# Kernel tuning notes

Measured on AMD Instinct MI355X. Metric: run time of the kernel, lower is better.

Reference implementation:

```python
import jax, jax.numpy as jnp
import numpy as np
from jax.ops import segment_sum

N = 100000   # nodes
E = 1600000  # edges
D = 128      # input feature dim
H = 128      # hidden dim
S = 64       # substructure ids
G = 512      # graphs in batch
EPS = 1e-5


def setup_inputs() -> dict:
    key = jax.random.key(0)
    ks = jax.random.split(key, 12)
    subst_ids = jax.random.randint(ks[0], (N,), 0, S)
    x = jax.random.normal(ks[1], (N, D), dtype=jnp.float32)
    # column 5 carries the integer substructure id, as in data.x[:, 5].long()
    x = x.at[:, 5].set(subst_ids.astype(jnp.float32))
    edge_index = jax.random.randint(ks[2], (2, E), 0, N)
    batch = jnp.sort(jax.random.randint(ks[3], (N,), 0, G))
    s = 0.05  # weight scale to keep activations sane
    return {
        "x": x,
        "edge_index": edge_index,
        "subst_ids": subst_ids,
        "batch": batch,
        "attn_w1": jax.random.normal(ks[4], (D, 64), jnp.float32) * s,
        "attn_b1": jnp.zeros((64,), jnp.float32),
        "attn_w2": jax.random.normal(ks[5], (64, 1), jnp.float32) * s,
        "conv_w0": jax.random.normal(ks[6], (D + 1, H), jnp.float32) * s,
        "conv_b0": jnp.zeros((H,), jnp.float32),
        "conv_w1": jax.random.normal(ks[7], (H, H), jnp.float32) * s,
        "conv_b1": jnp.zeros((H,), jnp.float32),
        "conv_w2": jax.random.normal(ks[8], (H, H), jnp.float32) * s,
        "conv_b2": jnp.zeros((H,), jnp.float32),
        "conv_w3": jax.random.normal(ks[9], (H, H), jnp.float32) * s,
        "conv_b3": jnp.zeros((H,), jnp.float32),
        "bn_gamma": jnp.ones((4, H), jnp.float32),
        "bn_beta": jnp.zeros((4, H), jnp.float32),
        "bn_rmean": jnp.zeros((4, H), jnp.float32),
        "bn_rvar": jnp.ones((4, H), jnp.float32),
        "head_w1": jax.random.normal(ks[10], (H, H // 2), jnp.float32) * s,
        "head_b1": jnp.zeros((H // 2,), jnp.float32),
        "head_w2": jax.random.normal(ks[11], (H // 2, 1), jnp.float32) * s,
        "head_b2": jnp.zeros((1,), jnp.float32),
    }


def _gcn_conv(x, src, dst, dinv, w, b):
    # PyG GCNConv with self-loops: out[dst] += d^-1/2_src d^-1/2_dst (xW)[src]
    h = x @ w                                   # [N, H]
    coef = dinv[src] * dinv[dst]                # [E]
    agg = segment_sum(h[src] * coef[:, None], dst, num_segments=N)
    agg = agg + h * (dinv * dinv)[:, None]      # self-loop term
    return agg + b


def reference(x, edge_index, subst_ids, batch,
              attn_w1, attn_b1, attn_w2,
              conv_w0, conv_b0, conv_w1, conv_b1, conv_w2, conv_b2, conv_w3, conv_b3,
              bn_gamma, bn_beta, bn_rmean, bn_rvar,
              head_w1, head_b1, head_w2, head_b2):
    # --- substructure attention ---
    ones_n = jnp.ones((N,), x.dtype)
    cnt = jnp.maximum(segment_sum(ones_n, subst_ids, num_segments=S), 1.0)
    subst_mean = segment_sum(x, subst_ids, num_segments=S) / cnt[:, None]  # [S, D]
    scores = jnp.tanh(subst_mean @ attn_w1 + attn_b1) @ attn_w2            # [S, 1]
    subst_attn = jax.nn.softmax(scores, axis=0)                            # [S, 1]
    atom_attn = subst_attn[subst_ids]                                      # [N, 1]
    h = jnp.concatenate([x, atom_attn], axis=1)                            # [N, D+1]

    # --- shared symmetric normalization (self-loops included) ---
    src, dst = edge_index[0], edge_index[1]
    deg = segment_sum(jnp.ones((E,), x.dtype), dst, num_segments=N) + 1.0
    dinv = jax.lax.rsqrt(deg)

    convs = [(conv_w0, conv_b0), (conv_w1, conv_b1), (conv_w2, conv_b2), (conv_w3, conv_b3)]
    for i, (w, b) in enumerate(convs):
        h = _gcn_conv(h, src, dst, dinv, w, b)
        # BatchNorm1d in eval mode
        h = (h - bn_rmean[i]) * jax.lax.rsqrt(bn_rvar[i] + EPS) * bn_gamma[i] + bn_beta[i]
        h = jax.nn.elu(h) if i < 3 else jax.nn.relu(h)
        # dropout p=0.3 is identity in inference

    # --- global mean pool over graphs ---
    gcnt = jnp.maximum(segment_sum(jnp.ones((N,), x.dtype), batch, num_segments=G), 1.0)
    pooled = segment_sum(h, batch, num_segments=G) / gcnt[:, None]         # [G, H]

    # --- prediction head (dropout off) ---
    z = jax.nn.elu(pooled @ head_w1 + head_b1)
    return z @ head_w2 + head_b2                                            # [G, 1]
```

## Files before the change

kernel.cpp:

```cpp
#include <hip/hip_runtime.h>
#include <cmath>

#define NN 100000
#define EE 1600000
#define DD 128
#define HH 128
#define SS 64
#define GG 512

typedef float f32x4 __attribute__((ext_vector_type(4)));
typedef short s16x8 __attribute__((ext_vector_type(8)));

constexpr size_t alignup(size_t x){ return (x + 255) & ~(size_t)255; }
constexpr size_t SZ_P16   = (size_t)NN*64*sizeof(unsigned);
constexpr size_t OFF_HW   = 0;
constexpr size_t OFF_H    = alignup(OFF_HW + SZ_P16);
constexpr size_t OFF_CSRS = alignup(OFF_H + SZ_P16);
constexpr size_t OFF_ROW  = alignup(OFF_CSRS + (size_t)EE*4);
constexpr size_t OFF_RANK = alignup(OFF_ROW + (size_t)(NN+1)*4);
constexpr size_t OFF_DINV = alignup(OFF_RANK + (size_t)EE*4);
constexpr size_t OFF_BSUM = alignup(OFF_DINV + (size_t)NN*4);
constexpr size_t OFF_BOFF = alignup(OFF_BSUM + 512*4);
constexpr size_t OFF_SATT = alignup(OFF_BOFF + 512*4);
constexpr size_t OFF_GST  = alignup(OFF_SATT + 64*4);
constexpr size_t OFF_BH   = alignup(OFF_GST + 513*4);
constexpr size_t OFF_BO   = alignup(OFF_BH + (size_t)64*400*4);
constexpr size_t OFF_TOT  = alignup(OFF_BO + (size_t)64*400*4);
constexpr size_t OFF_ROW2 = alignup(OFF_TOT + 64*4);
constexpr size_t OFF_LIST = alignup(OFF_ROW2 + 65*4);
constexpr size_t OFF_W16  = alignup(OFF_LIST + (size_t)NN*4);
constexpr size_t OFF_DEG  = alignup(OFF_W16 + (size_t)3*8192*4);
constexpr size_t OFF_POOL = alignup(OFF_DEG + (size_t)NN*4);
constexpr size_t OFF_GSUM = alignup(OFF_POOL + (size_t)GG*HH*4);
constexpr size_t OFF_END  = alignup(OFF_GSUM + (size_t)SS*DD*4);
constexpr size_t ZERO_BEG   = OFF_DEG;
constexpr size_t ZERO_BYTES = OFF_END - OFF_DEG;

__device__ __forceinline__ unsigned pack2bf(float a, float b){
  unsigned ua = __float_as_uint(a); ua += 0x7fffu + ((ua >> 16) & 1u);
  unsigned ub = __float_as_uint(b); ub += 0x7fffu + ((ub >> 16) & 1u);
  return (ua >> 16) | (ub & 0xffff0000u);
}
__device__ __forceinline__ float bf_lo(unsigned u){ return __uint_as_float(u << 16); }
__device__ __forceinline__ float bf_hi(unsigned u){ return __uint_as_float(u & 0xffff0000u); }
__device__ __forceinline__ s16x8 as_s16x8(uint4 v){ union { uint4 u; s16x8 s; } x; x.u = v; return x.s; }

__global__ __launch_bounds__(256) void hist_kernel(const int* __restrict__ sid, int* __restrict__ bhist)
{
  __shared__ int h[64];
  int t = threadIdx.x, b = blockIdx.x;
  if (t < 64) h[t] = 0;
  __syncthreads();
  int n = b*256 + t;
  if (n < NN) atomicAdd(&h[sid[n]], 1);
  __syncthreads();
  if (t < 64) bhist[t*400 + b] = h[t];
}

__global__ __launch_bounds__(512) void offs_kernel(const int* __restrict__ bhist, int* __restrict__ boff2, int* __restrict__ tots)
{
  __shared__ int sh[512];
  int s = blockIdx.x, t = threadIdx.x;
  int v = (t < 391) ? bhist[s*400 + t] : 0;
  sh[t] = v;
  __syncthreads();
  for (int off = 1; off < 512; off <<= 1) {
    int u = (t >= off) ? sh[t - off] : 0;
    __syncthreads();
    sh[t] += u;
    __syncthreads();
  }
  if (t < 391) boff2[s*400 + t] = sh[t] - v;
  if (t == 511) tots[s] = sh[511];
}

__global__ __launch_bounds__(64) void base_kernel(const int* __restrict__ tots, int* __restrict__ row2)
{
  int l = threadIdx.x;
  int v = tots[l];
  int xv = v;
  #pragma unroll
  for (int off = 1; off < 64; off <<= 1) {
    int u = __shfl_up(xv, off, 64);
    if (l >= off) xv += u;
  }
  row2[l] = xv - v;
  if (l == 63) row2[64] = xv;
}

__global__ __launch_bounds__(256) void fill2_kernel(
    const int* __restrict__ sid, const int* __restrict__ row2,
    const int* __restrict__ boff2, unsigned* __restrict__ list)
{
  __shared__ int h[64];
  int t = threadIdx.x, b = blockIdx.x;
  if (t < 64) h[t] = 0;
  __syncthreads();
  int n = b*256 + t;
  if (n < NN) {
    int s = sid[n];
    int lr = atomicAdd(&h[s], 1);
    int pos = row2[s] + boff2[s*400 + b] + lr;
    list[pos] = ((unsigned)s << 24) | (unsigned)n;
  }
}

__global__ __launch_bounds__(256) void subst_sum(
    const unsigned* __restrict__ list, const float* __restrict__ x,
    float* __restrict__ gsum)
{
  int b = blockIdx.x, t = threadIdx.x;
  int lane = t & 63, w = t >> 6;
  const int per = (NN + 1023)/1024;
  const int q   = (per + 3)/4;
  int bend = min(b*per + per, NN);
  int beg = b*per + w*q;
  int end = min(bend, beg + q);
  if (beg >= end) return;
  int d0 = lane * 2;
  float ax = 0.f, ay = 0.f;
  int scur = (int)(list[beg] >> 24);
  int i = beg;
  for (; i + 4 <= end; i += 4) {
    unsigned u0 = list[i], u1 = list[i+1], u2 = list[i+2], u3 = list[i+3];
    float2 v0 = *(const float2*)(x + (size_t)(u0 & 0xffffffu)*DD + d0);
    float2 v1 = *(const float2*)(x + (size_t)(u1 & 0xffffffu)*DD + d0);
    float2 v2 = *(const float2*)(x + (size_t)(u2 & 0xffffffu)*DD + d0);
    float2 v3 = *(const float2*)(x + (size_t)(u3 & 0xffffffu)*DD + d0);
    int s0 = u0 >> 24, s1 = u1 >> 24, s2 = u2 >> 24, s3 = u3 >> 24;
    if (s0 != scur) { atomicAdd(&gsum[scur*DD + d0], ax); atomicAdd(&gsum[scur*DD + d0 + 1], ay); scur = s0; ax = 0.f; ay = 0.f; }
    ax += v0.x; ay += v0.y;
    if (s1 != scur) { atomicAdd(&gsum[scur*DD + d0], ax); atomicAdd(&gsum[scur*DD + d0 + 1], ay); scur = s1; ax = 0.f; ay = 0.f; }
    ax += v1.x; ay += v1.y;
    if (s2 != scur) { atomicAdd(&gsum[scur*DD + d0], ax); atomicAdd(&gsum[scur*DD + d0 + 1], ay); scur = s2; ax = 0.f; ay = 0.f; }
    ax += v2.x; ay += v2.y;
    if (s3 != scur) { atomicAdd(&gsum[scur*DD + d0], ax); atomicAdd(&gsum[scur*DD + d0 + 1], ay); scur = s3; ax = 0.f; ay = 0.f; }
    ax += v3.x; ay += v3.y;
  }
  for (; i < end; ++i) {
    unsigned u = list[i];
    float2 v = *(const float2*)(x + (size_t)(u & 0xffffffu)*DD + d0);
    int s = u >> 24;
    if (s != scur) { atomicAdd(&gsum[scur*DD + d0], ax); atomicAdd(&gsum[scur*DD + d0 + 1], ay); scur = s; ax = 0.f; ay = 0.f; }
    ax += v.x; ay += v.y;
  }
  atomicAdd(&gsum[scur*DD + d0],     ax);
  atomicAdd(&gsum[scur*DD + d0 + 1], ay);
}

__global__ __launch_bounds__(64) void attn_kernel(
    const float* __restrict__ g_sum, const int* __restrict__ row2,
    const float* __restrict__ w1, const float* __restrict__ b1,
    const float* __restrict__ w2, float* __restrict__ subst_attn)
{
  __shared__ float mean[SS*130];
  __shared__ float sc[SS];
  __shared__ float es[SS];
  int t = threadIdx.x;
  for (int i = t; i < SS*DD; i += 64) {
    int s = i >> 7, d = i & 127;
    float c = fmaxf((float)(row2[s+1] - row2[s]), 1.0f);
    mean[s*130 + d] = g_sum[i] / c;
  }
  __syncthreads();
  float score = 0.0f;
  for (int j = 0; j < 64; ++j) {
    float a0 = 0, a1 = 0, a2 = 0, a3 = 0;
    for (int d = 0; d < DD; d += 4) {
      a0 += mean[t*130 + d    ] * w1[(d    )*64 + j];
      a1 += mean[t*130 + d + 1] * w1[(d + 1)*64 + j];
      a2 += mean[t*130 + d + 2] * w1[(d + 2)*64 + j];
      a3 += mean[t*130 + d + 3] * w1[(d + 3)*64 + j];
    }
    score += tanhf(a0 + a1 + a2 + a3 + b1[j]) * w2[j];
  }
  sc[t] = score;
  __syncthreads();
  float m = -1e30f;
  for (int i = 0; i < SS; ++i) m = fmaxf(m, sc[i]);
  float e = expf(score - m);
  es[t] = e;
  __syncthreads();
  float sum = 0.0f;
  for (int i = 0; i < SS; ++i) sum += es[i];
  subst_attn[t] = e / sum;
}

__global__ __launch_bounds__(256) void deg_rank_kernel(
    const int* __restrict__ dst, int* __restrict__ deg, int* __restrict__ rank)
{
  int e = blockIdx.x*256 + threadIdx.x;
  if (e < EE) rank[e] = atomicAdd(&deg[dst[e]], 1);
}

__global__ __launch_bounds__(256) void dinv_kernel(const int* __restrict__ deg, float* __restrict__ dinv)
{
  int n = blockIdx.x*256 + threadIdx.x;
  if (n < NN) dinv[n] = rsqrtf((float)(deg[n] + 1));
}

__global__ __launch_bounds__(256) void scan1(const int* __restrict__ deg, int* __restrict__ row_off, int* __restrict__ bsum)
{
  __shared__ int s[256];
  int tid = threadIdx.x;
  int n = blockIdx.x*256 + tid;
  int v = (n < NN) ? deg[n] : 0;
  s[tid] = v;
  __syncthreads();
  for (int off = 1; off < 256; off <<= 1) {
    int t = (tid >= off) ? s[tid - off] : 0;
    __syncthreads();
    s[tid] += t;
    __syncthreads();
  }
  if (n < NN) row_off[n] = s[tid] - v;
  if (tid == 255) bsum[blockIdx.x] = s[255];
}

__global__ __launch_bounds__(512) void scan2(const int* __restrict__ bsum, int* __restrict__ boff, int nb)
{
  __shared__ int s[512];
  int t = threadIdx.x;
  int v = (t < nb) ? bsum[t] : 0;
  s[t] = v;
  __syncthreads();
  for (int off = 1; off < 512; off <<= 1) {
    int u = (t >= off) ? s[t - off] : 0;
    __syncthreads();
    s[t] += u;
    __syncthreads();
  }
  boff[t] = s[t] - v;
}

__global__ __launch_bounds__(256) void scan3(int* __restrict__ row_off, const int* __restrict__ boff)
{
  int n = blockIdx.x*256 + threadIdx.x;
  if (n < NN) row_off[n] = row_off[n] + boff[n >> 8];
  if (n == 0) row_off[NN] = EE;
}

__global__ __launch_bounds__(256) void fill_kernel(
    const int* __restrict__ src, const int* __restrict__ dst,
    const int* __restrict__ rank, const int* __restrict__ row_off,
    int* __restrict__ csr_src)
{
  int e = blockIdx.x*256 + threadIdx.x;
  if (e >= EE) return;
  int d = dst[e];
  int pos = row_off[d] + rank[e];
  csr_src[pos] = src[e];
}

__global__ __launch_bounds__(256) void gemm_kernel(
    const float* __restrict__ A, const float* __restrict__ W,
    unsigned* __restrict__ out,
    const int* __restrict__ sid, const float* __restrict__ sattn, int layer0)
{
  __shared__ float sA[32][129];
  __shared__ float sW[32][128];
  __shared__ float sExtra[128];
  __shared__ float sAttn[128];
  int tid = threadIdx.x;
  int tx = tid & 15, ty = tid >> 4;
  int row0 = blockIdx.x * 128;

  if (layer0) {
    if (tid < 128) sExtra[tid] = W[128*128 + tid];
    if (tid < 128) {
      int n = row0 + tid;
      sAttn[tid] = (n < NN) ? sattn[sid[n]] : 0.0f;
    }
  }

  float acc[8][8];
  #pragma unroll
  for (int i = 0; i < 8; ++i)
    #pragma unroll
    for (int j = 0; j < 8; ++j) acc[i][j] = 0.0f;

  for (int k0 = 0; k0 < 128; k0 += 32) {
    __syncthreads();
    #pragma unroll
    for (int p = 0; p < 4; ++p) {
      int q  = tid + 256*p;
      int r  = q >> 3;
      int kk = (q & 7) << 2;
      int n = row0 + r;
      float4 v = make_float4(0.f, 0.f, 0.f, 0.f);
      if (n < NN) v = *(const float4*)(A + (size_t)n*128 + k0 + kk);
      sA[kk+0][r] = v.x; sA[kk+1][r] = v.y; sA[kk+2][r] = v.z; sA[kk+3][r] = v.w;
    }
    #pragma unroll
    for (int p = 0; p < 4; ++p) {
      int q  = tid + 256*p;
      int kr = q >> 5;
      int c  = (q & 31) << 2;
      float4 v = *(const float4*)(W + (size_t)(k0 + kr)*128 + c);
      *(float4*)&sW[kr][c] = v;
    }
    __syncthreads();
    #pragma unroll 4
    for (int kk = 0; kk < 32; ++kk) {
      float av[8], wv[8];
      #pragma unroll
      for (int i = 0; i < 8; ++i) av[i] = sA[kk][ty*8 + i];
      #pragma unroll
      for (int j = 0; j < 8; ++j) wv[j] = sW[kk][tx*8 + j];
      #pragma unroll
      for (int i = 0; i < 8; ++i)
        #pragma unroll
        for (int j = 0; j < 8; ++j)
          acc[i][j] += av[i] * wv[j];
    }
  }

  if (layer0) {
    #pragma unroll
    for (int i = 0; i < 8; ++i) {
      float a = sAttn[ty*8 + i];
      #pragma unroll
      for (int j = 0; j < 8; ++j) acc[i][j] += a * sExtra[tx*8 + j];
    }
  }

  #pragma unroll
  for (int i = 0; i < 8; ++i) {
    int n = row0 + ty*8 + i;
    if (n < NN) {
      uint4 pk;
      pk.x = pack2bf(acc[i][0], acc[i][1]);
      pk.y = pack2bf(acc[i][2], acc[i][3]);
      pk.z = pack2bf(acc[i][4], acc[i][5]);
      pk.w = pack2bf(acc[i][6], acc[i][7]);
      *(uint4*)(out + (size_t)n*64 + tx*4) = pk;
    }
  }
}

__global__ __launch_bounds__(256) void packw_kernel(const float* __restrict__ W, unsigned* __restrict__ W16)
{
  int q = blockIdx.x*256 + threadIdx.x;
  int c = q & 127, kp = q >> 7;
  float f0 = W[(size_t)(2*kp  )*128 + c];
  float f1 = W[(size_t)(2*kp+1)*128 + c];
  W16[c*64 + kp] = pack2bf(f0, f1);
}

__global__ __launch_bounds__(256) void gemm16_kernel(
    const unsigned* __restrict__ A16, const unsigned* __restrict__ W16,
    unsigned* __restrict__ out)
{
  __shared__ unsigned lds[16384];
  int tid = threadIdx.x;
  int lane = tid & 63;
  int row0 = blockIdx.x * 128;

  #pragma unroll
  for (int p = 0; p < 8; ++p) {
    int q  = tid + 256*p;
    int r  = q >> 4;
    int ch = q & 15;
    int n = row0 + r;
    uint4 v = make_uint4(0u,0u,0u,0u);
    if (n < NN) v = *(const uint4*)(A16 + (size_t)n*64 + ch*4);
    int idx = (r*64 + ch*4) ^ ((r & 7) << 2);
    *(uint4*)&lds[idx] = v;
  }
  {
    const uint4* w4 = (const uint4*)W16;
    #pragma unroll
    for (int p = 0; p < 8; ++p) {
      int ch = tid + 256*p;
      int base = ch*4;
      int c = base >> 6;
      int idx = 8192 + (base ^ ((c & 7) << 2));
      *(uint4*)&lds[idx] = w4[ch];
    }
  }
  __syncthreads();

  int w = tid >> 6;
  int wrow = w * 32;
  int swz = (lane & 7) << 2;
  int kgrp = (lane >> 4) * 4;

  f32x4 acc0[8], acc1[8];
  #pragma unroll
  for (int j = 0; j < 8; ++j) { acc0[j] = (f32x4){0,0,0,0}; acc1[j] = (f32x4){0,0,0,0}; }

  #pragma unroll
  for (int kk = 0; kk < 4; ++kk) {
    int kbase = kk*16 + kgrp;
    int rowA0 = wrow + (lane & 15);
    int rowA1 = wrow + 16 + (lane & 15);
    uint4 avu0 = *(const uint4*)&lds[(rowA0*64 + kbase) ^ swz];
    uint4 avu1 = *(const uint4*)&lds[(rowA1*64 + kbase) ^ swz];
    s16x8 a0 = as_s16x8(avu0);
    s16x8 a1 = as_s16x8(avu1);
    #pragma unroll
    for (int j = 0; j < 8; ++j) {
      int col = j*16 + (lane & 15);
      uint4 bvu = *(const uint4*)&lds[8192 + ((col*64 + kbase) ^ swz)];
      s16x8 bfr = as_s16x8(bvu);
      acc0[j] = __builtin_amdgcn_mfma_f32_16x16x32_bf16(a0, bfr, acc0[j], 0, 0, 0);
      acc1[j] = __builtin_amdgcn_mfma_f32_16x16x32_bf16(a1, bfr, acc1[j], 0, 0, 0);
    }
  }
  __syncthreads();

  #pragma unroll
  for (int i2 = 0; i2 < 2; ++i2) {
    #pragma unroll
    for (int j = 0; j < 8; ++j) {
      f32x4 v = i2 ? acc1[j] : acc0[j];
      #pragma unroll
      for (int reg = 0; reg < 4; ++reg) {
        float own = v[reg];
        float part = __shfl_xor(own, 1, 64);
        if ((lane & 1) == 0) {
          int r  = wrow + i2*16 + (lane >> 4)*4 + reg;
          int cp = j*8 + ((lane & 15) >> 1);
          lds[r*68 + cp] = pack2bf(own, part);
        }
      }
    }
  }
  __syncthreads();

  #pragma unroll
  for (int p = 0; p < 8; ++p) {
    int q  = tid + 256*p;
    int r  = q >> 4;
    int ch = q & 15;
    int n = row0 + r;
    if (n < NN) {
      uint4 v = *(const uint4*)&lds[r*68 + ch*4];
      *(uint4*)(out + (size_t)n*64 + ch*4) = v;
    }
  }
}

__global__ __launch_bounds__(256) void gather_kernel(
    const unsigned* __restrict__ hw, const int* __restrict__ row_off,
    const int* __restrict__ csr_src,
    const float* __restrict__ dinv, const float* __restrict__ bias,
    const float* __restrict__ gma, const float* __restrict__ bta,
    const float* __restrict__ rmn, const float* __restrict__ rvr,
    unsigned* __restrict__ out, int relu_act)
{
  int w = (blockIdx.x*256 + threadIdx.x) >> 6;
  int lane = threadIdx.x & 63;
  int n0 = w * 2;
  if (n0 >= NN) return;
  n0 = __builtin_amdgcn_readfirstlane(n0);
  int n1 = n0 + 1;
  int j0 = lane * 2;

  float di0 = dinv[n0], di1 = dinv[n1];
  unsigned su0 = hw[(size_t)n0*64 + lane];
  unsigned su1 = hw[(size_t)n1*64 + lane];
  float ax0 = bf_lo(su0)*di0*di0, ay0 = bf_hi(su0)*di0*di0;
  float ax1 = bf_lo(su1)*di1*di1, ay1 = bf_hi(su1)*di1*di1;

  int b0 = __builtin_amdgcn_readfirstlane(row_off[n0]);
  int e0 = __builtin_amdgcn_readfirstlane(row_off[n0+1]);
  int e1 = __builtin_amdgcn_readfirstlane(row_off[n1+1]);
  int i0 = b0, i1 = e0;

  for (; i0 + 4 <= e0 && i1 + 4 <= e1; i0 += 4, i1 += 4) {
    int s00 = csr_src[i0+0], s01 = csr_src[i0+1], s02 = csr_src[i0+2], s03 = csr_src[i0+3];
    int s10 = csr_src[i1+0], s11 = csr_src[i1+1], s12 = csr_src[i1+2], s13 = csr_src[i1+3];
    unsigned u00 = hw[(size_t)s00*64 + lane];
    unsigned u01 = hw[(size_t)s01*64 + lane];
    unsigned u02 = hw[(size_t)s02*64 + lane];
    unsigned u03 = hw[(size_t)s03*64 + lane];
    unsigned u10 = hw[(size_t)s10*64 + lane];
    unsigned u11 = hw[(size_t)s11*64 + lane];
    unsigned u12 = hw[(size_t)s12*64 + lane];
    unsigned u13 = hw[(size_t)s13*64 + lane];
    float c00 = dinv[s00]*di0, c01 = dinv[s01]*di0, c02 = dinv[s02]*di0, c03 = dinv[s03]*di0;
    float c10 = dinv[s10]*di1, c11 = dinv[s11]*di1, c12 = dinv[s12]*di1, c13 = dinv[s13]*di1;
    ax0 += bf_lo(u00)*c00 + bf_lo(u01)*c01 + bf_lo(u02)*c02 + bf_lo(u03)*c03;
    ay0 += bf_hi(u00)*c00 + bf_hi(u01)*c01 + bf_hi(u02)*c02 + bf_hi(u03)*c03;
    ax1 += bf_lo(u10)*c10 + bf_lo(u11)*c11 + bf_lo(u12)*c12 + bf_lo(u13)*c13;
    ay1 += bf_hi(u10)*c10 + bf_hi(u11)*c11 + bf_hi(u12)*c12 + bf_hi(u13)*c13;
  }
  for (; i0 + 4 <= e0; i0 += 4) {
    int s0 = csr_src[i0+0], s1 = csr_src[i0+1], s2 = csr_src[i0+2], s3 = csr_src[i0+3];
    unsigned u0 = hw[(size_t)s0*64 + lane];
    unsigned u1 = hw[(size_t)s1*64 + lane];
    unsigned u2 = hw[(size_t)s2*64 + lane];
    unsigned u3 = hw[(size_t)s3*64 + lane];
    float c0 = dinv[s0]*di0, c1 = dinv[s1]*di0, c2 = dinv[s2]*di0, c3 = dinv[s3]*di0;
    ax0 += bf_lo(u0)*c0 + bf_lo(u1)*c1 + bf_lo(u2)*c2 + bf_lo(u3)*c3;
    ay0 += bf_hi(u0)*c0 + bf_hi(u1)*c1 + bf_hi(u2)*c2 + bf_hi(u3)*c3;
  }
  for (; i1 + 4 <= e1; i1 += 4) {
    int s0 = csr_src[i1+0], s1 = csr_src[i1+1], s2 = csr_src[i1+2], s3 = csr_src[i1+3];
    unsigned u0 = hw[(size_t)s0*64 + lane];
    unsigned u1 = hw[(size_t)s1*64 + lane];
    unsigned u2 = hw[(size_t)s2*64 + lane];
    unsigned u3 = hw[(size_t)s3*64 + lane];
    float c0 = dinv[s0]*di1, c1 = dinv[s1]*di1, c2 = dinv[s2]*di1, c3 = dinv[s3]*di1;
    ax1 += bf_lo(u0)*c0 + bf_lo(u1)*c1 + bf_lo(u2)*c2 + bf_lo(u3)*c3;
    ay1 += bf_hi(u0)*c0 + bf_hi(u1)*c1 + bf_hi(u2)*c2 + bf_hi(u3)*c3;
  }
  for (; i0 < e0; ++i0) {
    int s = csr_src[i0];
    float c = dinv[s]*di0;
    unsigned u = hw[(size_t)s*64 + lane];
    ax0 += bf_lo(u)*c; ay0 += bf_hi(u)*c;
  }
  for (; i1 < e1; ++i1) {
    int s = csr_src[i1];
    float c = dinv[s]*di1;
    unsigned u = hw[(size_t)s*64 + lane];
    ax1 += bf_lo(u)*c; ay1 += bf_hi(u)*c;
  }

  float iv0 = rsqrtf(rvr[j0]   + 1e-5f);
  float iv1 = rsqrtf(rvr[j0+1] + 1e-5f);
  float g0 = gma[j0], g1 = gma[j0+1];
  float m0 = rmn[j0], m1 = rmn[j0+1];
  float t0 = bta[j0], t1 = bta[j0+1];
  float bb0 = bias[j0], bb1 = bias[j0+1];

  float y00 = (ax0 + bb0 - m0) * iv0 * g0 + t0;
  float y01 = (ay0 + bb1 - m1) * iv1 * g1 + t1;
  float y10 = (ax1 + bb0 - m0) * iv0 * g0 + t0;
  float y11 = (ay1 + bb1 - m1) * iv1 * g1 + t1;
  if (relu_act) {
    y00 = fmaxf(y00, 0.0f); y01 = fmaxf(y01, 0.0f);
    y10 = fmaxf(y10, 0.0f); y11 = fmaxf(y11, 0.0f);
  } else {
    y00 = (y00 > 0.0f) ? y00 : expm1f(y00);
    y01 = (y01 > 0.0f) ? y01 : expm1f(y01);
    y10 = (y10 > 0.0f) ? y10 : expm1f(y10);
    y11 = (y11 > 0.0f) ? y11 : expm1f(y11);
  }
  out[(size_t)n0*64 + lane] = pack2bf(y00, y01);
  out[(size_t)n1*64 + lane] = pack2bf(y10, y11);
}

__global__ __launch_bounds__(256) void gstart_kernel(const int* __restrict__ batch, int* __restrict__ start)
{
  int n = blockIdx.x*256 + threadIdx.x;
  if (n >= NN) return;
  int b  = batch[n];
  int bp = (n == 0) ? -1 : batch[n-1];
  for (int g = bp + 1; g <= b; ++g) start[g] = n;
  if (n == NN-1) {
    for (int g = b + 1; g <= GG; ++g) start[g] = NN;
  }
}

__global__ __launch_bounds__(256) void pool_kernel(
    const unsigned* __restrict__ h16, const int* __restrict__ batch, float* __restrict__ pooled)
{
  int wave = (blockIdx.x*256 + threadIdx.x) >> 6;
  int lane = threadIdx.x & 63;
  const int CH = 64;
  int beg = wave * CH;
  if (beg >= NN) return;
  int end = min(beg + CH, NN);
  int j0 = lane * 2;
  float ax = 0.f, ay = 0.f;
  int gcur = batch[beg];
  for (int n = beg; n < end; ++n) {
    int g = batch[n];
    if (g != gcur) {
      atomicAdd(&pooled[(size_t)gcur*128 + j0],     ax);
      atomicAdd(&pooled[(size_t)gcur*128 + j0 + 1], ay);
      ax = 0.f; ay = 0.f; gcur = g;
    }
    unsigned u = h16[(size_t)n*64 + lane];
    ax += bf_lo(u); ay += bf_hi(u);
  }
  atomicAdd(&pooled[(size_t)gcur*128 + j0],     ax);
  atomicAdd(&pooled[(size_t)gcur*128 + j0 + 1], ay);
}

__global__ __launch_bounds__(64) void head_kernel(
    const float* __restrict__ pooled, const int* __restrict__ start,
    const float* __restrict__ w1, const float* __restrict__ b1,
    const float* __restrict__ w2, const float* __restrict__ b2,
    float* __restrict__ out)
{
  __shared__ float p[128];
  int g = blockIdx.x;
  int t = threadIdx.x;
  float cnt = fmaxf((float)(start[g+1] - start[g]), 1.0f);
  p[t]      = pooled[(size_t)g*128 + t]      / cnt;
  p[t + 64] = pooled[(size_t)g*128 + t + 64] / cnt;
  __syncthreads();
  float a = 0.f;
  #pragma unroll 4
  for (int d = 0; d < 128; ++d) a += p[d] * w1[d*64 + t];
  float z = a + b1[t];
  z = (z > 0.f) ? z : expm1f(z);
  float v = z * w2[t];
  #pragma unroll
  for (int off = 32; off > 0; off >>= 1) v += __shfl_down(v, off, 64);
  if (t == 0) out[g] = v + b2[0];
}

extern "C" void kernel_launch(void* const* d_in, const int* in_sizes, int n_in,
                              void* d_out, int out_size, void* d_ws, size_t ws_size,
                              hipStream_t stream)
{
  const float* x        = (const float*)d_in[0];
  const int*   eidx     = (const int*)d_in[1];
  const int*   sid      = (const int*)d_in[2];
  const int*   batch    = (const int*)d_in[3];
  const float* attn_w1  = (const float*)d_in[4];
  const float* attn_b1  = (const float*)d_in[5];
  const float* attn_w2  = (const float*)d_in[6];
  const float* conv_w[4] = {(const float*)d_in[7], (const float*)d_in[9],
                            (const float*)d_in[11], (const float*)d_in[13]};
  const float* conv_b[4] = {(const float*)d_in[8], (const float*)d_in[10],
                            (const float*)d_in[12], (const float*)d_in[14]};
  const float* bn_gamma = (const float*)d_in[15];
  const float* bn_beta  = (const float*)d_in[16];
  const float* bn_rmean = (const float*)d_in[17];
  const float* bn_rvar  = (const float*)d_in[18];
  const float* head_w1  = (const float*)d_in[19];
  const float* head_b1  = (const float*)d_in[20];
  const float* head_w2  = (const float*)d_in[21];
  const float* head_b2  = (const float*)d_in[22];
  float* out = (float*)d_out;

  char* ws = (char*)d_ws;
  unsigned* hw16  = (unsigned*)(ws + OFF_HW);
  unsigned* h16   = (unsigned*)(ws + OFF_H);
  int*   csr_src  = (int*)  (ws + OFF_CSRS);
  int*   row_off  = (int*)  (ws + OFF_ROW);
  int*   rank     = (int*)  (ws + OFF_RANK);
  float* dinv     = (float*)(ws + OFF_DINV);
  int*   bsum     = (int*)  (ws + OFF_BSUM);
  int*   boff     = (int*)  (ws + OFF_BOFF);
  float* sattn    = (float*)(ws + OFF_SATT);
  int*   gstart   = (int*)  (ws + OFF_GST);
  int*   bhist    = (int*)  (ws + OFF_BH);
  int*   boff2    = (int*)  (ws + OFF_BO);
  int*   tots     = (int*)  (ws + OFF_TOT);
  int*   row2     = (int*)  (ws + OFF_ROW2);
  unsigned* list  = (unsigned*)(ws + OFF_LIST);
  unsigned* w16   = (unsigned*)(ws + OFF_W16);
  int*   deg      = (int*)  (ws + OFF_DEG);
  float* pooled   = (float*)(ws + OFF_POOL);
  float* gsum     = (float*)(ws + OFF_GSUM);

  const int* e_src = eidx;
  const int* e_dst = eidx + EE;

  hipMemsetAsync(ws + ZERO_BEG, 0, ZERO_BYTES, stream);

  int nb256 = (NN + 255)/256;
  hist_kernel <<<nb256, 256, 0, stream>>>(sid, bhist);
  offs_kernel <<<64, 512, 0, stream>>>(bhist, boff2, tots);
  base_kernel <<<1, 64, 0, stream>>>(tots, row2);
  fill2_kernel<<<nb256, 256, 0, stream>>>(sid, row2, boff2, list);
  subst_sum   <<<1024, 256, 0, stream>>>(list, x, gsum);
  attn_kernel <<<1, 64, 0, stream>>>(gsum, row2, attn_w1, attn_b1, attn_w2, sattn);

  deg_rank_kernel<<<(EE + 255)/256, 256, 0, stream>>>(e_dst, deg, rank);
  dinv_kernel<<<nb256, 256, 0, stream>>>(deg, dinv);
  scan1<<<nb256, 256, 0, stream>>>(deg, row_off, bsum);
  scan2<<<1, 512, 0, stream>>>(bsum, boff, nb256);
  scan3<<<nb256, 256, 0, stream>>>(row_off, boff);
  fill_kernel<<<(EE + 255)/256, 256, 0, stream>>>(e_src, e_dst, rank, row_off, csr_src);

  gstart_kernel<<<nb256, 256, 0, stream>>>(batch, gstart);

  for (int L = 1; L < 4; ++L)
    packw_kernel<<<32, 256, 0, stream>>>(conv_w[L], w16 + (size_t)(L-1)*8192);

  int gemm_grid = (NN + 127)/128;
  int gat_grid  = ((NN/2)*64 + 255)/256;
  for (int L = 0; L < 4; ++L) {
    if (L == 0)
      gemm_kernel<<<gemm_grid, 256, 0, stream>>>(x, conv_w[0], hw16, sid, sattn, 1);
    else
      gemm16_kernel<<<gemm_grid, 256, 0, stream>>>(h16, w16 + (size_t)(L-1)*8192, hw16);
    gather_kernel<<<gat_grid, 256, 0, stream>>>(hw16, row_off, csr_src, dinv,
        conv_b[L], bn_gamma + L*HH, bn_beta + L*HH, bn_rmean + L*HH, bn_rvar + L*HH,
        h16, (L == 3) ? 1 : 0);
  }

  int pool_waves  = (NN + 63)/64;
  int pool_blocks = (pool_waves + 3)/4;
  pool_kernel<<<pool_blocks, 256, 0, stream>>>(h16, batch, pooled);
  head_kernel<<<GG, 64, 0, stream>>>(pooled, gstart, head_w1, head_b1, head_w2, head_b2, out);
}
```

Baseline: 624.2 us.

## Build CSR via two-level bucketed radix scatter and parallelize attention kernel

Replaces the global-atomic degree/rank CSR build with a two-pass bucketed scheme. Edges are first histogrammed and scattered into 196 buckets of 512 destination nodes using shared-memory atomics. Each bucket is then sorted into CSR within one block, which also computes row offsets and dinv. This is meant to remove contended global atomics and random scattered writes, at the cost of extra intermediate arrays and more passes over the edge list. The attention MLP kernel also moves from 64 to 1024 threads, with weights staged in shared memory and a shuffle reduction.

Result: faster. 537.8 us (-13.8%).

```diff
diff --git a/kernel.cpp b/kernel.cpp
--- a/kernel.cpp
+++ b/kernel.cpp
@@ -8,6 +8,10 @@
 #define SS 64
 #define GG 512
 
+#define NBE 782
+#define EBK 196
+#define EHS 800
+
 typedef float f32x4 __attribute__((ext_vector_type(4)));
 typedef short s16x8 __attribute__((ext_vector_type(8)));
 
@@ -17,11 +21,8 @@
 constexpr size_t OFF_H    = alignup(OFF_HW + SZ_P16);
 constexpr size_t OFF_CSRS = alignup(OFF_H + SZ_P16);
 constexpr size_t OFF_ROW  = alignup(OFF_CSRS + (size_t)EE*4);
-constexpr size_t OFF_RANK = alignup(OFF_ROW + (size_t)(NN+1)*4);
-constexpr size_t OFF_DINV = alignup(OFF_RANK + (size_t)EE*4);
-constexpr size_t OFF_BSUM = alignup(OFF_DINV + (size_t)NN*4);
-constexpr size_t OFF_BOFF = alignup(OFF_BSUM + 512*4);
-constexpr size_t OFF_SATT = alignup(OFF_BOFF + 512*4);
+constexpr size_t OFF_DINV = alignup(OFF_ROW + (size_t)(NN+1)*4);
+constexpr size_t OFF_SATT = alignup(OFF_DINV + (size_t)NN*4);
 constexpr size_t OFF_GST  = alignup(OFF_SATT + 64*4);
 constexpr size_t OFF_BH   = alignup(OFF_GST + 513*4);
 constexpr size_t OFF_BO   = alignup(OFF_BH + (size_t)64*400*4);
@@ -29,12 +30,17 @@
 constexpr size_t OFF_ROW2 = alignup(OFF_TOT + 64*4);
 constexpr size_t OFF_LIST = alignup(OFF_ROW2 + 65*4);
 constexpr size_t OFF_W16  = alignup(OFF_LIST + (size_t)NN*4);
-constexpr size_t OFF_DEG  = alignup(OFF_W16 + (size_t)3*8192*4);
-constexpr size_t OFF_POOL = alignup(OFF_DEG + (size_t)NN*4);
+constexpr size_t OFF_EH   = alignup(OFF_W16 + (size_t)3*8192*4);
+constexpr size_t OFF_EB   = alignup(OFF_EH + (size_t)EBK*EHS*4);
+constexpr size_t OFF_ET   = alignup(OFF_EB + (size_t)EBK*EHS*4);
+constexpr size_t OFF_EBASE= alignup(OFF_ET + EBK*4);
+constexpr size_t OFF_DSTE = alignup(OFF_EBASE + 200*4);
+constexpr size_t OFF_SRCE = alignup(OFF_DSTE + (size_t)EE*4);
+constexpr size_t OFF_POOL = alignup(OFF_SRCE + (size_t)EE*4);
 constexpr size_t OFF_GSUM = alignup(OFF_POOL + (size_t)GG*HH*4);
 constexpr size_t OFF_END  = alignup(OFF_GSUM + (size_t)SS*DD*4);
-constexpr size_t ZERO_BEG   = OFF_DEG;
-constexpr size_t ZERO_BYTES = OFF_END - OFF_DEG;
+constexpr size_t ZERO_BEG   = OFF_POOL;
+constexpr size_t ZERO_BYTES = OFF_END - OFF_POOL;
 
 __device__ __forceinline__ unsigned pack2bf(float a, float b){
   unsigned ua = __float_as_uint(a); ua += 0x7fffu + ((ua >> 16) & 1u);
@@ -148,108 +154,165 @@
   atomicAdd(&gsum[scur*DD + d0 + 1], ay);
 }
 
-__global__ __launch_bounds__(64) void attn_kernel(
+__global__ __launch_bounds__(1024) void attn_kernel(
     const float* __restrict__ g_sum, const int* __restrict__ row2,
     const float* __restrict__ w1, const float* __restrict__ b1,
     const float* __restrict__ w2, float* __restrict__ subst_attn)
 {
-  __shared__ float mean[SS*130];
+  __shared__ float smean[SS*130];
+  __shared__ float sw1[8192];
   __shared__ float sc[SS];
-  __shared__ float es[SS];
   int t = threadIdx.x;
-  for (int i = t; i < SS*DD; i += 64) {
+  for (int i = t; i < SS*DD; i += 1024) {
     int s = i >> 7, d = i & 127;
     float c = fmaxf((float)(row2[s+1] - row2[s]), 1.0f);
-    mean[s*130 + d] = g_sum[i] / c;
-  }
-  __syncthreads();
-  float score = 0.0f;
-  for (int j = 0; j < 64; ++j) {
-    float a0 = 0, a1 = 0, a2 = 0, a3 = 0;
-    for (int d = 0; d < DD; d += 4) {
-      a0 += mean[t*130 + d    ] * w1[(d    )*64 + j];
-      a1 += mean[t*130 + d + 1] * w1[(d + 1)*64 + j];
-      a2 += mean[t*130 + d + 2] * w1[(d + 2)*64 + j];
-      a3 += mean[t*130 + d + 3] * w1[(d + 3)*64 + j];
-    }
-    score += tanhf(a0 + a1 + a2 + a3 + b1[j]) * w2[j];
-  }
-  sc[t] = score;
-  __syncthreads();
-  float m = -1e30f;
-  for (int i = 0; i < SS; ++i) m = fmaxf(m, sc[i]);
-  float e = expf(score - m);
-  es[t] = e;
-  __syncthreads();
-  float sum = 0.0f;
-  for (int i = 0; i < SS; ++i) sum += es[i];
-  subst_attn[t] = e / sum;
-}
-
-__global__ __launch_bounds__(256) void deg_rank_kernel(
-    const int* __restrict__ dst, int* __restrict__ deg, int* __restrict__ rank)
-{
-  int e = blockIdx.x*256 + threadIdx.x;
-  if (e < EE) rank[e] = atomicAdd(&deg[dst[e]], 1);
-}
-
-__global__ __launch_bounds__(256) void dinv_kernel(const int* __restrict__ deg, float* __restrict__ dinv)
-{
-  int n = blockIdx.x*256 + threadIdx.x;
-  if (n < NN) dinv[n] = rsqrtf((float)(deg[n] + 1));
-}
-
-__global__ __launch_bounds__(256) void scan1(const int* __restrict__ deg, int* __restrict__ row_off, int* __restrict__ bsum)
-{
-  __shared__ int s[256];
-  int tid = threadIdx.x;
-  int n = blockIdx.x*256 + tid;
-  int v = (n < NN) ? deg[n] : 0;
-  s[tid] = v;
+    smean[s*130 + d] = g_sum[i] / c;
+  }
+  for (int i = t; i < 8192; i += 1024) sw1[i] = w1[i];
+  __syncthreads();
+
+  int s = t >> 4, jq = t & 15;
+  float a0 = 0, a1 = 0, a2 = 0, a3 = 0;
+  #pragma unroll 4
+  for (int d = 0; d < 128; ++d) {
+    float m = smean[s*130 + d];
+    a0 += m * sw1[d*64 + jq     ];
+    a1 += m * sw1[d*64 + jq + 16];
+    a2 += m * sw1[d*64 + jq + 32];
+    a3 += m * sw1[d*64 + jq + 48];
+  }
+  float acc = tanhf(a0 + b1[jq     ]) * w2[jq     ]
+            + tanhf(a1 + b1[jq + 16]) * w2[jq + 16]
+            + tanhf(a2 + b1[jq + 32]) * w2[jq + 32]
+            + tanhf(a3 + b1[jq + 48]) * w2[jq + 48];
+  acc += __shfl_xor(acc, 1, 64);
+  acc += __shfl_xor(acc, 2, 64);
+  acc += __shfl_xor(acc, 4, 64);
+  acc += __shfl_xor(acc, 8, 64);
+  if (jq == 0) sc[s] = acc;
+  __syncthreads();
+  if (t < 64) {
+    float score = sc[t];
+    float m = -1e30f;
+    for (int i = 0; i < SS; ++i) m = fmaxf(m, sc[i]);
+    float e = expf(score - m);
+    float sum = 0.0f;
+    for (int i = 0; i < SS; ++i) sum += expf(sc[i] - m);
+    subst_attn[t] = e / sum;
+  }
+}
+
+__global__ __launch_bounds__(256) void ehist_kernel(const int* __restrict__ dst, int* __restrict__ ehist)
+{
+  __shared__ int h[EBK];
+  int t = threadIdx.x, b = blockIdx.x;
+  if (t < EBK) h[t] = 0;
+  __syncthreads();
+  #pragma unroll
+  for (int ii = 0; ii < 8; ++ii) {
+    int e = b*2048 + ii*256 + t;
+    if (e < EE) atomicAdd(&h[dst[e] >> 9], 1);
+  }
+  __syncthreads();
+  if (t < EBK) ehist[t*EHS + b] = h[t];
+}
+
+__global__ __launch_bounds__(1024) void eoffs_kernel(const int* __restrict__ ehist, int* __restrict__ eboff, int* __restrict__ etots)
+{
+  __shared__ int sh[1024];
+  int s = blockIdx.x, t = threadIdx.x;
+  int v = (t < NBE) ? ehist[s*EHS + t] : 0;
+  sh[t] = v;
+  __syncthreads();
+  for (int off = 1; off < 1024; off <<= 1) {
+    int u = (t >= off) ? sh[t - off] : 0;
+    __syncthreads();
+    sh[t] += u;
+    __syncthreads();
+  }
+  if (t < NBE) eboff[s*EHS + t] = sh[t] - v;
+  if (t == 1023) etots[s] = sh[1023];
+}
+
+__global__ __launch_bounds__(256) void ebase_kernel(const int* __restrict__ etots, int* __restrict__ ebase)
+{
+  __shared__ int sh[256];
+  int t = threadIdx.x;
+  int v = (t < EBK) ? etots[t] : 0;
+  sh[t] = v;
   __syncthreads();
   for (int off = 1; off < 256; off <<= 1) {
-    int t = (tid >= off) ? s[tid - off] : 0;
-    __syncthreads();
-    s[tid] += t;
-    __syncthreads();
-  }
-  if (n < NN) row_off[n] = s[tid] - v;
-  if (tid == 255) bsum[blockIdx.x] = s[255];
-}
-
-__global__ __launch_bounds__(512) void scan2(const int* __restrict__ bsum, int* __restrict__ boff, int nb)
-{
-  __shared__ int s[512];
-  int t = threadIdx.x;
-  int v = (t < nb) ? bsum[t] : 0;
-  s[t] = v;
+    int u = (t >= off) ? sh[t - off] : 0;
+    __syncthreads();
+    sh[t] += u;
+    __syncthreads();
+  }
+  if (t < EBK) ebase[t] = sh[t] - v;
+  if (t == EBK-1) ebase[EBK] = sh[t];
+}
+
+__global__ __launch_bounds__(256) void escat_kernel(
+    const int* __restrict__ src, const int* __restrict__ dst,
+    const int* __restrict__ ebase, const int* __restrict__ eboff,
+    int* __restrict__ dste, int* __restrict__ srce)
+{
+  __shared__ int h[EBK];
+  int t = threadIdx.x, b = blockIdx.x;
+  if (t < EBK) h[t] = 0;
+  __syncthreads();
+  #pragma unroll
+  for (int ii = 0; ii < 8; ++ii) {
+    int e = b*2048 + ii*256 + t;
+    if (e < EE) {
+      int d = dst[e];
+      int k = d >> 9;
+      int lr = atomicAdd(&h[k], 1);
+      int pos = ebase[k] + eboff[k*EHS + b] + lr;
+      dste[pos] = d;
+      srce[pos] = src[e];
+    }
+  }
+}
+
+__global__ __launch_bounds__(1024) void csr_build(
+    const int* __restrict__ ebase, const int* __restrict__ dste, const int* __restrict__ srce,
+    int* __restrict__ row_off, float* __restrict__ dinv, int* __restrict__ csr_src)
+{
+  __shared__ int scnt[512];
+  __shared__ int sh[512];
+  __shared__ int cur[512];
+  int b = blockIdx.x, t = threadIdx.x;
+  int base = ebase[b], cnt_b = ebase[b+1] - base;
+  if (t < 512) scnt[t] = 0;
+  __syncthreads();
+  for (int i = t; i < cnt_b; i += 1024)
+    atomicAdd(&scnt[dste[base + i] & 511], 1);
+  __syncthreads();
+  int orig = (t < 512) ? scnt[t] : 0;
+  if (t < 512) sh[t] = orig;
   __syncthreads();
   for (int off = 1; off < 512; off <<= 1) {
-    int u = (t >= off) ? s[t - off] : 0;
-    __syncthreads();
-    s[t] += u;
-    __syncthreads();
-  }
-  boff[t] = s[t] - v;
-}
-
-__global__ __launch_bounds__(256) void scan3(int* __restrict__ row_off, const int* __restrict__ boff)
-{
-  int n = blockIdx.x*256 + threadIdx.x;
-  if (n < NN) row_off[n] = row_off[n] + boff[n >> 8];
-  if (n == 0) row_off[NN] = EE;
-}
-
-__global__ __launch_bounds__(256) void fill_kernel(
-    const int* __restrict__ src, const int* __restrict__ dst,
-    const int* __restrict__ rank, const int* __restrict__ row_off,
-    int* __restrict__ csr_src)
-{
-  int e = blockIdx.x*256 + threadIdx.x;
-  if (e >= EE) return;
-  int d = dst[e];
-  int pos = row_off[d] + rank[e];
-  csr_src[pos] = src[e];
+    int u = (t < 512 && t >= off) ? sh[t - off] : 0;
+    __syncthreads();
+    if (t < 512) sh[t] += u;
+    __syncthreads();
+  }
+  if (t < 512) {
+    int excl = sh[t] - orig;
+    int n = b*512 + t;
+    if (n < NN) {
+      row_off[n] = base + excl;
+      dinv[n] = rsqrtf((float)(orig + 1));
+    }
+    cur[t] = excl;
+  }
+  if (b == EBK-1 && t == 0) row_off[NN] = EE;
+  __syncthreads();
+  for (int i = t; i < cnt_b; i += 1024) {
+    int dl = dste[base + i] & 511;
+    int pos = atomicAdd(&cur[dl], 1);
+    csr_src[base + pos] = srce[base + i];
+  }
 }
 
 __global__ __launch_bounds__(256) void gemm_kernel(
@@ -635,10 +698,7 @@
   unsigned* h16   = (unsigned*)(ws + OFF_H);
   int*   csr_src  = (int*)  (ws + OFF_CSRS);
   int*   row_off  = (int*)  (ws + OFF_ROW);
-  int*   rank     = (int*)  (ws + OFF_RANK);
   float* dinv     = (float*)(ws + OFF_DINV);
-  int*   bsum     = (int*)  (ws + OFF_BSUM);
-  int*   boff     = (int*)  (ws + OFF_BOFF);
   float* sattn    = (float*)(ws + OFF_SATT);
   int*   gstart   = (int*)  (ws + OFF_GST);
   int*   bhist    = (int*)  (ws + OFF_BH);
@@ -647,7 +707,12 @@
   int*   row2     = (int*)  (ws + OFF_ROW2);
   unsigned* list  = (unsigned*)(ws + OFF_LIST);
   unsigned* w16   = (unsigned*)(ws + OFF_W16);
-  int*   deg      = (int*)  (ws + OFF_DEG);
+  int*   ehist    = (int*)  (ws + OFF_EH);
+  int*   eboff    = (int*)  (ws + OFF_EB);
+  int*   etots    = (int*)  (ws + OFF_ET);
+  int*   ebase    = (int*)  (ws + OFF_EBASE);
+  int*   dste     = (int*)  (ws + OFF_DSTE);
+  int*   srce     = (int*)  (ws + OFF_SRCE);
   float* pooled   = (float*)(ws + OFF_POOL);
   float* gsum     = (float*)(ws + OFF_GSUM);
 
@@ -657,19 +722,19 @@
   hipMemsetAsync(ws + ZERO_BEG, 0, ZERO_BYTES, stream);
 
   int nb256 = (NN + 255)/256;
+
   hist_kernel <<<nb256, 256, 0, stream>>>(sid, bhist);
   offs_kernel <<<64, 512, 0, stream>>>(bhist, boff2, tots);
   base_kernel <<<1, 64, 0, stream>>>(tots, row2);
   fill2_kernel<<<nb256, 256, 0, stream>>>(sid, row2, boff2, list);
   subst_sum   <<<1024, 256, 0, stream>>>(list, x, gsum);
-  attn_kernel <<<1, 64, 0, stream>>>(gsum, row2, attn_w1, attn_b1, attn_w2, sattn);
-
-  deg_rank_kernel<<<(EE + 255)/256, 256, 0, stream>>>(e_dst, deg, rank);
-  dinv_kernel<<<nb256, 256, 0, stream>>>(deg, dinv);
-  scan1<<<nb256, 256, 0, stream>>>(deg, row_off, bsum);
-  scan2<<<1, 512, 0, stream>>>(bsum, boff, nb256);
-  scan3<<<nb256, 256, 0, stream>>>(row_off, boff);
-  fill_kernel<<<(EE + 255)/256, 256, 0, stream>>>(e_src, e_dst, rank, row_off, csr_src);
+  attn_kernel <<<1, 1024, 0, stream>>>(gsum, row2, attn_w1, attn_b1, attn_w2, sattn);
+
+  ehist_kernel<<<NBE, 256, 0, stream>>>(e_dst, ehist);
+  eoffs_kernel<<<EBK, 1024, 0, stream>>>(ehist, eboff, etots);
+  ebase_kernel<<<1, 256, 0, stream>>>(etots, ebase);
+  escat_kernel<<<NBE, 256, 0, stream>>>(e_src, e_dst, ebase, eboff, dste, srce);
+  csr_build   <<<EBK, 1024, 0, stream>>>(ebase, dste, srce, row_off, dinv, csr_src);
 
   gstart_kernel<<<nb256, 256, 0, stream>>>(batch, gstart);
 
```
